# Kernel tuning notes

Hardware: AMD Instinct MI355X
Metric: run time of the kernel (lower is better)

Reference implementation:

```python
import math
import jax, jax.numpy as jnp
import numpy as np

EMBED_DIM = 512
NUM_HEADS = 8
PROJ_DIM = EMBED_DIM // NUM_HEADS
ATTN_WINDOW = 5
HALF_WINDOW = (ATTN_WINDOW - 1) // 2  # 2
ATTN_PARAM = 1.0
ATTN_DISPLACEMENT = 1
# per-head positions: ['center','left','right','center'] repeated to 8 heads (synst repeats short lists)
HEAD_SHIFTS = np.array([0, -ATTN_DISPLACEMENT, ATTN_DISPLACEMENT, 0] * 2, dtype=np.int32)


def _xavier(key, shape):
    fan_in, fan_out = shape[1], shape[0]
    bound = math.sqrt(6.0 / (fan_in + fan_out))
    return jax.random.uniform(key, shape, jnp.float32, -bound, bound)


def setup_inputs() -> dict:
    key = jax.random.key(0)
    k1, k2, k3, k4, k5 = jax.random.split(key, 5)
    B, S, E = 8, 4096, EMBED_DIM
    return {
        "values": jax.random.normal(k1, (B, S, E), jnp.float32),
        "keys": jax.random.normal(k2, (B, S, E), jnp.float32),
        "queries": jax.random.normal(k3, (B, S, E), jnp.float32),
        "input_weights": _xavier(k4, (E, E)),        # value projection (attn_weights=1, non-learned type)
        "out_proj_w": _xavier(k5, (E, E)),           # output_projection.weight (bias=False)
    }


def reference(values, keys, queries, input_weights, out_proj_w):
    # keys/queries are unused by the hard-coded 'normal' attention path (no QK^T)
    B, S, E = values.shape
    H, Dh, hw, W = NUM_HEADS, PROJ_DIM, HALF_WINDOW, ATTN_WINDOW

    # value projection + head split: [B,S,E] -> [B,H,S,Dh]
    v = values @ input_weights.T
    v = v.reshape(B, S, H, Dh).transpose(0, 2, 1, 3)

    # fixed Gaussian filter over relative distances [-hw, hw] (unnormalized pdf, as in the source)
    dist = jnp.arange(-hw, hw + 1, dtype=jnp.float32)
    filt = (1.0 / (ATTN_PARAM * math.sqrt(2.0 * math.pi))) * jnp.exp(-0.5 * (dist / ATTN_PARAM) ** 2)  # [W]

    shifts = jnp.asarray(HEAD_SHIFTS)            # [H] per-head center displacement
    P = hw + int(np.max(np.abs(HEAD_SHIFTS)))    # pad so all gathers are in range
    vp = jnp.pad(v, ((0, 0), (0, 0), (P, P), (0, 0)))  # [B,H,S+2P,Dh]

    h_ar = jnp.arange(H)[:, None]                # [H,1]
    pos = jnp.arange(S)[None, :]                 # [1,S]
    out = jnp.zeros_like(v)
    for j in range(W):                           # tiny fixed window loop (W=5)
        idx = pos + P + shifts[:, None] + (j - hw)   # [H,S]
        out = out + filt[j] * vp[:, h_ar, idx, :]    # [B,H,S,Dh]

    out = out.transpose(0, 2, 1, 3).reshape(B, S, E)
    return out @ out_proj_w.T
```

## Files before the change

kernel.cpp:

```cpp
#include <hip/hip_runtime.h>
#include <hip/hip_bf16.h>
#include <stdint.h>

typedef __bf16 bf16;
typedef __bf16 bf16x8 __attribute__((ext_vector_type(8)));
typedef float  f32x4  __attribute__((ext_vector_type(4)));

#define BM 128
#define BN 128
#define BK 32
#define E  512
#define SB 4112
#define M1 (8 * SB)
#define M2 32768

__device__ __forceinline__ void gl_lds_16(const bf16* g, bf16* l) {
    __builtin_amdgcn_global_load_lds(
        (__attribute__((address_space(1))) void*)g,
        (__attribute__((address_space(3))) void*)l,
        16, 0, 0);
}

__global__ __launch_bounds__(256)
void gemm_bt_bf16(const bf16* __restrict__ A, const bf16* __restrict__ Bm,
                  bf16* __restrict__ C, int M, int N, int K)
{
    __shared__ bf16 As[BM * BK];
    __shared__ bf16 Bs[BN * BK];

    const int tid  = threadIdx.x;
    const int bm   = blockIdx.x;
    const int bn   = blockIdx.y;
    const int wave = tid >> 6;
    const int lane = tid & 63;
    const int wm   = wave >> 1;
    const int wn   = wave & 1;

    const int srow = tid >> 2;
    const int scol = (tid & 3) << 3;
    const size_t a_off = (size_t)(bm * BM + srow) * K + scol;
    const size_t b_off = (size_t)(bn * BN + srow) * K + scol;
    const int    l_off = srow * BK + scol;

    f32x4 acc[4][4] = {};
    const int fr = lane & 15;
    const int ks = (lane >> 4) << 3;

    for (int k0 = 0; k0 < K; k0 += BK) {
        gl_lds_16(A  + a_off + k0,                  As + l_off);
        gl_lds_16(A  + a_off + (size_t)64 * K + k0, As + l_off + 64 * BK);
        gl_lds_16(Bm + b_off + k0,                  Bs + l_off);
        gl_lds_16(Bm + b_off + (size_t)64 * K + k0, Bs + l_off + 64 * BK);
        __syncthreads();

        bf16x8 af[4], bfr[4];
#pragma unroll
        for (int i = 0; i < 4; ++i) {
            af[i]  = *(const bf16x8*)(As + (wm * 64 + i * 16 + fr) * BK + ks);
            bfr[i] = *(const bf16x8*)(Bs + (wn * 64 + i * 16 + fr) * BK + ks);
        }
#pragma unroll
        for (int i = 0; i < 4; ++i)
#pragma unroll
            for (int j = 0; j < 4; ++j)
                acc[i][j] = __builtin_amdgcn_mfma_f32_16x16x32_bf16(af[i], bfr[j], acc[i][j], 0, 0, 0);
        __syncthreads();
    }

    const int crow = (lane >> 4) << 2;
    const int ccol = lane & 15;
    const int row0 = bm * BM + wm * 64 + crow;
    const int col0 = bn * BN + wn * 64 + ccol;
#pragma unroll
    for (int i = 0; i < 4; ++i)
#pragma unroll
        for (int j = 0; j < 4; ++j)
#pragma unroll
            for (int r = 0; r < 4; ++r)
                C[(size_t)(row0 + i * 16 + r) * N + (col0 + j * 16)] = (bf16)acc[i][j][r];
}

__global__ __launch_bounds__(256)
void gemm2_gather(const bf16* __restrict__ P, const bf16* __restrict__ Bm,
                  float* __restrict__ C)
{
    __shared__ bf16 As[BM * BK];
    __shared__ bf16 Bs[BN * BK];

    const int tid  = threadIdx.x;
    const int bm   = blockIdx.x;
    const int bn   = blockIdx.y;
    const int wave = tid >> 6;
    const int lane = tid & 63;
    const int wm   = wave >> 1;
    const int wn   = wave & 1;

    const int srow = tid >> 2;
    const int scol = (tid & 3) << 3;

    const int m0 = bm * BM + srow;
    const int m1 = m0 + 64;
    const int prow0 = (m0 >> 12) * SB + (m0 & 4095) + 1;
    const int prow1 = (m1 >> 12) * SB + (m1 & 4095) + 1;

    const size_t b_off = (size_t)(bn * BN + srow) * E + scol;
    const int    l_off = srow * BK + scol;

    f32x4 acc[4][4] = {};
    const int fr = lane & 15;
    const int ks = (lane >> 4) << 3;

    for (int k0 = 0; k0 < E; k0 += BK) {
        const int h3 = (k0 >> 6) & 3;
        const int sh = (h3 == 1) ? -1 : (h3 == 2) ? 1 : 0;
        gl_lds_16(P + (size_t)(prow0 + sh) * E + scol + k0, As + l_off);
        gl_lds_16(P + (size_t)(prow1 + sh) * E + scol + k0, As + l_off + 64 * BK);
        gl_lds_16(Bm + b_off + k0,                          Bs + l_off);
        gl_lds_16(Bm + b_off + (size_t)64 * E + k0,         Bs + l_off + 64 * BK);
        __syncthreads();

        bf16x8 af[4], bfr[4];
#pragma unroll
        for (int i = 0; i < 4; ++i) {
            af[i]  = *(const bf16x8*)(As + (wm * 64 + i * 16 + fr) * BK + ks);
            bfr[i] = *(const bf16x8*)(Bs + (wn * 64 + i * 16 + fr) * BK + ks);
        }
#pragma unroll
        for (int i = 0; i < 4; ++i)
#pragma unroll
            for (int j = 0; j < 4; ++j)
                acc[i][j] = __builtin_amdgcn_mfma_f32_16x16x32_bf16(af[i], bfr[j], acc[i][j], 0, 0, 0);
        __syncthreads();
    }

    const int crow = (lane >> 4) << 2;
    const int ccol = lane & 15;
    const int row0 = bm * BM + wm * 64 + crow;
    const int col0 = bn * BN + wn * 64 + ccol;
#pragma unroll
    for (int i = 0; i < 4; ++i)
#pragma unroll
        for (int j = 0; j < 4; ++j)
#pragma unroll
            for (int r = 0; r < 4; ++r)
                C[(size_t)(row0 + i * 16 + r) * E + (col0 + j * 16)] = acc[i][j][r];
}

__global__ __launch_bounds__(256)
void prefilter(const float* __restrict__ vals, bf16* __restrict__ vg)
{
    const int idx = blockIdx.x * 256 + threadIdx.x;
    const int e8  = idx & 63;
    const int m   = idx >> 6;
    const int b   = m / SB;
    const int r   = m - b * SB;

    const float filt[5] = {0.05399096651318806f, 0.24197072451914337f,
                           0.3989422804014327f,
                           0.24197072451914337f, 0.05399096651318806f};
    float acc[8] = {0.f, 0.f, 0.f, 0.f, 0.f, 0.f, 0.f, 0.f};
    if (r < 4098) {
#pragma unroll
        for (int j = 0; j < 5; ++j) {
            const int sp = r - 3 + j;
            if (sp >= 0 && sp < 4096) {
                const f32x4* p = (const f32x4*)(vals + ((size_t)(b * 4096 + sp)) * E + e8 * 8);
                f32x4 x0 = p[0], x1 = p[1];
                const float w = filt[j];
                acc[0] += w * x0[0]; acc[1] += w * x0[1];
                acc[2] += w * x0[2]; acc[3] += w * x0[3];
                acc[4] += w * x1[0]; acc[5] += w * x1[1];
                acc[6] += w * x1[2]; acc[7] += w * x1[3];
            }
        }
    }
    bf16x8 o;
#pragma unroll
    for (int d = 0; d < 8; ++d) o[d] = (bf16)acc[d];
    *((bf16x8*)vg + idx) = o;
}

__global__ __launch_bounds__(256)
void cvt_weights(const float* __restrict__ w_in, const float* __restrict__ w_out,
                 bf16* __restrict__ win_b, bf16* __restrict__ wout_b)
{
    const int i = blockIdx.x * 256 + threadIdx.x;
    const int half = (E * E) / 8;
    const float* src = (i < half) ? w_in : w_out;
    bf16* dst        = (i < half) ? win_b : wout_b;
    const int k = (i < half) ? i : i - half;
    const f32x4* p = (const f32x4*)src + 2 * (size_t)k;
    f32x4 a = p[0], bq = p[1];
    bf16x8 o;
    o[0] = (bf16)a[0]; o[1] = (bf16)a[1]; o[2] = (bf16)a[2]; o[3] = (bf16)a[3];
    o[4] = (bf16)bq[0]; o[5] = (bf16)bq[1]; o[6] = (bf16)bq[2]; o[7] = (bf16)bq[3];
    *((bf16x8*)dst + k) = o;
}

extern "C" void kernel_launch(void* const* d_in, const int* in_sizes, int n_in,
                              void* d_out, int out_size, void* d_ws, size_t ws_size,
                              hipStream_t stream)
{
    const float* values = (const float*)d_in[0];
    const float* w_in   = (const float*)d_in[3];
    const float* w_out  = (const float*)d_in[4];
    float* out = (float*)d_out;

    bf16* win_b  = (bf16*)d_ws;
    bf16* wout_b = win_b + E * E;
    bf16* vg     = wout_b + E * E;
    bf16* Pbuf   = vg + (size_t)M1 * E;

    cvt_weights<<<(2 * E * E / 8) / 256, 256, 0, stream>>>(w_in, w_out, win_b, wout_b);
    prefilter<<<(size_t)M1 * 64 / 256, 256, 0, stream>>>(values, vg);

    dim3 g1(M1 / BM, E / BN);
    gemm_bt_bf16<<<g1, 256, 0, stream>>>(vg, win_b, Pbuf, M1, E, E);

    dim3 g2(M2 / BM, E / BN);
    gemm2_gather<<<g2, 256, 0, stream>>>(Pbuf, wout_b, out);
}
```

Baseline: 257.1 us.

## Merge GEMMs into weight-resident template with register-prefetched A fragments

Replaces the two LDS-tiled GEMM kernels with one templated kernel. Each block loads a 64-column slice of the weight (full K) into LDS once. Each wave streams its own A rows straight from global memory into registers, prefetching one k-step ahead, so the per-k-step barriers go away. The intermediate prefiltered buffer now lives in the output buffer to save workspace, and the row stride per batch is padded to 4128 so it divides into 256-row tiles. In exchange, A is read uncoalesced per lane with no LDS sharing across N tiles, and the larger LDS footprint limits occupancy.

```diff
diff --git a/kernel.cpp b/kernel.cpp
--- a/kernel.cpp
+++ b/kernel.cpp
@@ -6,160 +6,108 @@
 typedef __bf16 bf16x8 __attribute__((ext_vector_type(8)));
 typedef float  f32x4  __attribute__((ext_vector_type(4)));
 
-#define BM 128
-#define BN 128
-#define BK 32
-#define E  512
-#define SB 4112
-#define M1 (8 * SB)
-#define M2 32768
+#define E   512
+#define SB  4128
+#define M1  (8 * SB)
+#define M2  32768
 
 __device__ __forceinline__ void gl_lds_16(const bf16* g, bf16* l) {
     __builtin_amdgcn_global_load_lds(
         (__attribute__((address_space(1))) void*)g,
-        (__attribute__((address_space(3))) void*)l,
-        16, 0, 0);
+        (__attribute__((address_space(3))) void*)l, 16, 0, 0);
 }
 
-__global__ __launch_bounds__(256)
-void gemm_bt_bf16(const bf16* __restrict__ A, const bf16* __restrict__ Bm,
-                  bf16* __restrict__ C, int M, int N, int K)
+template<int GATHER, int OUT_BF16>
+__global__ __launch_bounds__(256, 2)
+void gemm_wres(const bf16* __restrict__ A, const bf16* __restrict__ W,
+               bf16* __restrict__ Cb, float* __restrict__ Cf)
 {
-    __shared__ bf16 As[BM * BK];
-    __shared__ bf16 Bs[BN * BK];
+    __shared__ bf16 Ws[16 * 2048];
+    const int tid  = threadIdx.x;
+    const int bn   = blockIdx.x;
+    const int bm   = blockIdx.y;
+    const int wave = tid >> 6, lane = tid & 63;
+    const int n0   = bn * 64;
 
-    const int tid  = threadIdx.x;
-    const int bm   = blockIdx.x;
-    const int bn   = blockIdx.y;
-    const int wave = tid >> 6;
-    const int lane = tid & 63;
-    const int wm   = wave >> 1;
-    const int wn   = wave & 1;
+#pragma unroll
+    for (int i = 0; i < 16; ++i) {
+        const int c  = i * 256 + tid;
+        const int kt = c >> 8;
+        const int r  = (c >> 2) & 63;
+        const int kc = (c & 3) << 3;
+        gl_lds_16(W + (size_t)(n0 + r) * E + (kt << 5) + kc, Ws + c * 8);
+    }
+    __syncthreads();
 
-    const int srow = tid >> 2;
-    const int scol = (tid & 3) << 3;
-    const size_t a_off = (size_t)(bm * BM + srow) * K + scol;
-    const size_t b_off = (size_t)(bn * BN + srow) * K + scol;
-    const int    l_off = srow * BK + scol;
+    const int fr = lane & 15, ks = (lane >> 4) << 3;
+    const int mbase = bm * 256 + wave * 64;
 
     f32x4 acc[4][4] = {};
-    const int fr = lane & 15;
-    const int ks = (lane >> 4) << 3;
 
-    for (int k0 = 0; k0 < K; k0 += BK) {
-        gl_lds_16(A  + a_off + k0,                  As + l_off);
-        gl_lds_16(A  + a_off + (size_t)64 * K + k0, As + l_off + 64 * BK);
-        gl_lds_16(Bm + b_off + k0,                  Bs + l_off);
-        gl_lds_16(Bm + b_off + (size_t)64 * K + k0, Bs + l_off + 64 * BK);
-        __syncthreads();
+    long arow[4];
+#pragma unroll
+    for (int i = 0; i < 4; ++i) {
+        const int m = mbase + i * 16 + fr;
+        arow[i] = GATHER ? (long)((m >> 12) * SB + (m & 4095) + 1) : (long)m;
+    }
 
-        bf16x8 af[4], bfr[4];
+    bf16x8 a_cur[4], a_nxt[4];
 #pragma unroll
-        for (int i = 0; i < 4; ++i) {
-            af[i]  = *(const bf16x8*)(As + (wm * 64 + i * 16 + fr) * BK + ks);
-            bfr[i] = *(const bf16x8*)(Bs + (wn * 64 + i * 16 + fr) * BK + ks);
+    for (int i = 0; i < 4; ++i)
+        a_cur[i] = *(const bf16x8*)(A + arow[i] * E + ks);
+
+#pragma unroll
+    for (int kt = 0; kt < 16; ++kt) {
+        if (kt < 15) {
+            const int k0n = (kt + 1) * 32;
+            int sh = 0;
+            if (GATHER) { const int h3 = (k0n >> 6) & 3; sh = (h3 == 1) ? -1 : (h3 == 2) ? 1 : 0; }
+#pragma unroll
+            for (int i = 0; i < 4; ++i)
+                a_nxt[i] = *(const bf16x8*)(A + (arow[i] + sh) * E + k0n + ks);
         }
+        bf16x8 bfrg[4];
+#pragma unroll
+        for (int j = 0; j < 4; ++j)
+            bfrg[j] = *(const bf16x8*)(Ws + kt * 2048 + (j * 16 + fr) * 32 + ks);
 #pragma unroll
         for (int i = 0; i < 4; ++i)
 #pragma unroll
             for (int j = 0; j < 4; ++j)
-                acc[i][j] = __builtin_amdgcn_mfma_f32_16x16x32_bf16(af[i], bfr[j], acc[i][j], 0, 0, 0);
-        __syncthreads();
+                acc[i][j] = __builtin_amdgcn_mfma_f32_16x16x32_bf16(a_cur[i], bfrg[j], acc[i][j], 0, 0, 0);
+#pragma unroll
+        for (int i = 0; i < 4; ++i) a_cur[i] = a_nxt[i];
     }
 
     const int crow = (lane >> 4) << 2;
     const int ccol = lane & 15;
-    const int row0 = bm * BM + wm * 64 + crow;
-    const int col0 = bn * BN + wn * 64 + ccol;
+    const int row0 = mbase + crow;
+    const int col0 = n0 + ccol;
 #pragma unroll
     for (int i = 0; i < 4; ++i)
 #pragma unroll
         for (int j = 0; j < 4; ++j)
 #pragma unroll
-            for (int r = 0; r < 4; ++r)
-                C[(size_t)(row0 + i * 16 + r) * N + (col0 + j * 16)] = (bf16)acc[i][j][r];
-}
-
-__global__ __launch_bounds__(256)
-void gemm2_gather(const bf16* __restrict__ P, const bf16* __restrict__ Bm,
-                  float* __restrict__ C)
-{
-    __shared__ bf16 As[BM * BK];
-    __shared__ bf16 Bs[BN * BK];
-
-    const int tid  = threadIdx.x;
-    const int bm   = blockIdx.x;
-    const int bn   = blockIdx.y;
-    const int wave = tid >> 6;
-    const int lane = tid & 63;
-    const int wm   = wave >> 1;
-    const int wn   = wave & 1;
-
-    const int srow = tid >> 2;
-    const int scol = (tid & 3) << 3;
-
-    const int m0 = bm * BM + srow;
-    const int m1 = m0 + 64;
-    const int prow0 = (m0 >> 12) * SB + (m0 & 4095) + 1;
-    const int prow1 = (m1 >> 12) * SB + (m1 & 4095) + 1;
-
-    const size_t b_off = (size_t)(bn * BN + srow) * E + scol;
-    const int    l_off = srow * BK + scol;
-
-    f32x4 acc[4][4] = {};
-    const int fr = lane & 15;
-    const int ks = (lane >> 4) << 3;
-
-    for (int k0 = 0; k0 < E; k0 += BK) {
-        const int h3 = (k0 >> 6) & 3;
-        const int sh = (h3 == 1) ? -1 : (h3 == 2) ? 1 : 0;
-        gl_lds_16(P + (size_t)(prow0 + sh) * E + scol + k0, As + l_off);
-        gl_lds_16(P + (size_t)(prow1 + sh) * E + scol + k0, As + l_off + 64 * BK);
-        gl_lds_16(Bm + b_off + k0,                          Bs + l_off);
-        gl_lds_16(Bm + b_off + (size_t)64 * E + k0,         Bs + l_off + 64 * BK);
-        __syncthreads();
-
-        bf16x8 af[4], bfr[4];
-#pragma unroll
-        for (int i = 0; i < 4; ++i) {
-            af[i]  = *(const bf16x8*)(As + (wm * 64 + i * 16 + fr) * BK + ks);
-            bfr[i] = *(const bf16x8*)(Bs + (wn * 64 + i * 16 + fr) * BK + ks);
-        }
-#pragma unroll
-        for (int i = 0; i < 4; ++i)
-#pragma unroll
-            for (int j = 0; j < 4; ++j)
-                acc[i][j] = __builtin_amdgcn_mfma_f32_16x16x32_bf16(af[i], bfr[j], acc[i][j], 0, 0, 0);
-        __syncthreads();
-    }
-
-    const int crow = (lane >> 4) << 2;
-    const int ccol = lane & 15;
-    const int row0 = bm * BM + wm * 64 + crow;
-    const int col0 = bn * BN + wn * 64 + ccol;
-#pragma unroll
-    for (int i = 0; i < 4; ++i)
-#pragma unroll
-        for (int j = 0; j < 4; ++j)
-#pragma unroll
-            for (int r = 0; r < 4; ++r)
-                C[(size_t)(row0 + i * 16 + r) * E + (col0 + j * 16)] = acc[i][j][r];
+            for (int r = 0; r < 4; ++r) {
+                const size_t idx = (size_t)(row0 + i * 16 + r) * E + (col0 + j * 16);
+                if (OUT_BF16) Cb[idx] = (bf16)acc[i][j][r];
+                else          Cf[idx] = acc[i][j][r];
+            }
 }
 
 __global__ __launch_bounds__(256)
 void prefilter(const float* __restrict__ vals, bf16* __restrict__ vg)
 {
+    const int b   = blockIdx.y;
     const int idx = blockIdx.x * 256 + threadIdx.x;
     const int e8  = idx & 63;
-    const int m   = idx >> 6;
-    const int b   = m / SB;
-    const int r   = m - b * SB;
+    const int r   = idx >> 6;
 
-    const float filt[5] = {0.05399096651318806f, 0.24197072451914337f,
-                           0.3989422804014327f,
-                           0.24197072451914337f, 0.05399096651318806f};
     float acc[8] = {0.f, 0.f, 0.f, 0.f, 0.f, 0.f, 0.f, 0.f};
     if (r < 4098) {
+        const float filt[5] = {0.05399096651318806f, 0.24197072451914337f,
+                               0.3989422804014327f,
+                               0.24197072451914337f, 0.05399096651318806f};
 #pragma unroll
         for (int j = 0; j < 5; ++j) {
             const int sp = r - 3 + j;
@@ -177,7 +125,7 @@
     bf16x8 o;
 #pragma unroll
     for (int d = 0; d < 8; ++d) o[d] = (bf16)acc[d];
-    *((bf16x8*)vg + idx) = o;
+    ((bf16x8*)vg)[(size_t)b * (SB * 64) + idx] = o;
 }
 
 __global__ __launch_bounds__(256)
@@ -208,15 +156,12 @@
 
     bf16* win_b  = (bf16*)d_ws;
     bf16* wout_b = win_b + E * E;
-    bf16* vg     = wout_b + E * E;
-    bf16* Pbuf   = vg + (size_t)M1 * E;
+    bf16* Pbuf   = wout_b + E * E;
+    bf16* vg     = (bf16*)d_out;
 
     cvt_weights<<<(2 * E * E / 8) / 256, 256, 0, stream>>>(w_in, w_out, win_b, wout_b);
-    prefilter<<<(size_t)M1 * 64 / 256, 256, 0, stream>>>(values, vg);
+    prefilter<<<dim3(SB * 64 / 256, 8), 256, 0, stream>>>(values, vg);
 
-    dim3 g1(M1 / BM, E / BN);
-    gemm_bt_bf16<<<g1, 256, 0, stream>>>(vg, win_b, Pbuf, M1, E, E);
-
-    dim3 g2(M2 / BM, E / BN);
-    gemm2_gather<<<g2, 256, 0, stream>>>(Pbuf, wout_b, out);
+    gemm_wres<0, 1><<<dim3(8, M1 / 256), 256, 0, stream>>>(vg, win_b, Pbuf, nullptr);
+    gemm_wres<1, 0><<<dim3(8, M2 / 256), 256, 0, stream>>>(Pbuf, wout_b, nullptr, out);
 }
```

Measured after the change: 291.4 us. +13.3%, slower.
